# Optimization experiments

Hardware: AMD Instinct MI355X
Metric: run time of the kernel (lower is better)

The kernel has to match this reference:

```python
import jax, jax.numpy as jnp
import numpy as np

H = 16  # headNum
D = 1024  # d_model
DK = D // H


def setup_inputs() -> dict:
    key = jax.random.key(0)
    ks = jax.random.split(key, 11)
    B, S = 2, 2048
    scale = 1.0 / np.sqrt(D)
    inp = {
        'query': jax.random.normal(ks[0], (B, S, D), jnp.float32),
        'key':   jax.random.normal(ks[1], (B, S, D), jnp.float32),
        'value': jax.random.normal(ks[2], (B, S, D), jnp.float32),
        # nn.Linear params: W is [out, in], y = x @ W.T + b
        'Wq': jax.random.normal(ks[3], (D, D), jnp.float32) * scale,
        'bq': jnp.zeros((D,), jnp.float32),
        'Wk': jax.random.normal(ks[4], (D, D), jnp.float32) * scale,
        'bk': jnp.zeros((D,), jnp.float32),
        'Wv': jax.random.normal(ks[5], (D, D), jnp.float32) * scale,
        'bv': jnp.zeros((D,), jnp.float32),
        'Wo': jax.random.normal(ks[6], (D, D), jnp.float32) * scale,
        'bo': jnp.zeros((D,), jnp.float32),
    }
    return inp


def reference(query, key, value, Wq, bq, Wk, bk, Wv, bv, Wo, bo):
    B, S, _ = query.shape
    # projections (torch Linear: x @ W.T + b), split heads -> [B, H, S, DK]
    q = (query @ Wq.T + bq).reshape(B, S, H, DK).transpose(0, 2, 1, 3)
    k = (key   @ Wk.T + bk).reshape(B, S, H, DK).transpose(0, 2, 1, 3)
    v = (value @ Wv.T + bv).reshape(B, S, H, DK).transpose(0, 2, 1, 3)
    # scores [B, H, S, S] = Q K^T / sqrt(d_k)  (fully materialized, as in source)
    scores = jnp.einsum('bhqd,bhkd->bhqk', q, k) * (DK ** -0.5)
    p_attn = jax.nn.softmax(scores, axis=-1)  # dropout = identity (eval)
    x = jnp.einsum('bhqk,bhkd->bhqd', p_attn, v)
    x = x.transpose(0, 2, 1, 3).reshape(B, S, H * DK)
    return x @ Wo.T + bo
```

## Files before the change

### kernel.cpp

```cpp
#include <hip/hip_runtime.h>

#define BATCH 2
#define SEQ   2048
#define NH    16
#define DK    64
#define DM    1024
#define MROWS 4096
#define NX    4194304
#define NW    1048576

typedef __attribute__((ext_vector_type(8))) short bf16x8;
typedef __attribute__((ext_vector_type(4))) short bf16x4;
typedef __attribute__((ext_vector_type(4))) float f32x4;
typedef __attribute__((ext_vector_type(4))) unsigned short us16x4;
typedef __attribute__((ext_vector_type(2))) unsigned int u32x2;

#if __has_builtin(__builtin_amdgcn_mfma_f32_16x16x16bf16_1k)
#define MFMA16(a, b, c) __builtin_amdgcn_mfma_f32_16x16x16bf16_1k(a, b, c, 0, 0, 0)
#else
#define MFMA16(a, b, c) (c)
#endif

__device__ __forceinline__ unsigned short f2bf(float f) {
  unsigned int u = __builtin_bit_cast(unsigned int, f);
  u += 0x7FFFu + ((u >> 16) & 1u);
  return (unsigned short)(u >> 16);
}

__device__ __forceinline__ unsigned int pkbf(float hi, float lo) {
#if __has_builtin(__builtin_amdgcn_perm)
  return __builtin_amdgcn_perm(__builtin_bit_cast(unsigned int, hi),
                               __builtin_bit_cast(unsigned int, lo), 0x07060302u);
#else
  return (__builtin_bit_cast(unsigned int, hi) & 0xffff0000u) |
         (__builtin_bit_cast(unsigned int, lo) >> 16);
#endif
}

__device__ __forceinline__ void g2l16(void* lds, const void* g) {
  __builtin_amdgcn_global_load_lds(
      (const __attribute__((address_space(1))) void*)g,
      (__attribute__((address_space(3))) void*)lds, 16, 0, 0);
}

__global__ __launch_bounds__(256) void cast_all(
    const float* __restrict__ q, const float* __restrict__ k, const float* __restrict__ v,
    const float* __restrict__ wq, const float* __restrict__ wk,
    const float* __restrict__ wv, const float* __restrict__ wo,
    unsigned short* __restrict__ dst) {
  size_t e = ((size_t)blockIdx.x * 256 + threadIdx.x) * 4;
  const float* src;
  if      (e < (size_t)NX)        src = q  + e;
  else if (e < (size_t)2*NX)      src = k  + (e - (size_t)NX);
  else if (e < (size_t)3*NX)      src = v  + (e - (size_t)2*NX);
  else if (e < (size_t)3*NX+NW)   src = wq + (e - (size_t)3*NX);
  else if (e < (size_t)3*NX+2*NW) src = wk + (e - (size_t)3*NX-NW);
  else if (e < (size_t)3*NX+3*NW) src = wv + (e - (size_t)3*NX-2*NW);
  else                            src = wo + (e - (size_t)3*NX-3*NW);
  float4 f = *(const float4*)src;
  us16x4 o;
  o[0] = f2bf(f.x); o[1] = f2bf(f.y); o[2] = f2bf(f.z); o[3] = f2bf(f.w);
  *(us16x4*)(dst + e) = o;
}

template <int MODE, int BM>
__global__ __launch_bounds__(256) void gemm_bt(
    const unsigned short* __restrict__ Xbase, const unsigned short* __restrict__ Wbase,
    const float* __restrict__ b0, const float* __restrict__ b1, const float* __restrict__ b2,
    unsigned short* __restrict__ qkv_dst, float* __restrict__ fout, float qscale) {
  constexpr int IM = BM / 32;
  constexpr int ASHOTS = (BM * 32) / 2048;
  const int tid  = threadIdx.x;
  const int lane = tid & 63;
  const int w    = tid >> 6;
  const int wm   = w >> 1, wn = w & 1;
  const int x15  = lane & 15, quad = lane >> 4;
  const int row0 = blockIdx.x * BM;
  const int col0 = blockIdx.y * 128;
  const int z    = blockIdx.z;

  const unsigned short* A  = Xbase + (size_t)z * NX;
  const unsigned short* Wp = Wbase + (size_t)z * NW;
  const float* bias = (MODE == 0) ? (z == 0 ? b0 : (z == 1 ? b1 : b2)) : b0;
  const float zs = (MODE == 0 && z == 0) ? qscale : 1.0f;

  __shared__ __align__(16) unsigned short At[2][BM * 32];
  __shared__ __align__(16) unsigned short Bt[2][128 * 32];

  f32x4 acc[IM][4] = {};

  auto stage = [&](int buf, int kt) {
#pragma unroll
    for (int j = 0; j < ASHOTS; ++j) {
      int e = (j * 256 + tid) * 8;
      int r = e >> 5, c = e & 31;
      g2l16(&At[buf][e], A + (size_t)(row0 + r) * DM + kt + c);
    }
#pragma unroll
    for (int j = 0; j < 2; ++j) {
      int e = (j * 256 + tid) * 8;
      int r = e >> 5, c = e & 31;
      g2l16(&Bt[buf][e], Wp + (size_t)(col0 + r) * DM + kt + c);
    }
  };

  stage(0, 0);
  for (int it = 0; it < DM / 32; ++it) {
    const int cur = it & 1;
    __syncthreads();
    if (it + 1 < DM / 32) stage(cur ^ 1, (it + 1) * 32);
    bf16x8 af[IM], bfv[4];
#pragma unroll
    for (int i = 0; i < IM; ++i)
      af[i] = *(const bf16x8*)&At[cur][(wm * (BM / 2) + i * 16 + x15) * 32 + quad * 8];
#pragma unroll
    for (int jn = 0; jn < 4; ++jn)
      bfv[jn] = *(const bf16x8*)&Bt[cur][(wn * 64 + jn * 16 + x15) * 32 + quad * 8];
#pragma unroll
    for (int i = 0; i < IM; ++i)
#pragma unroll
      for (int jn = 0; jn < 4; ++jn)
        acc[i][jn] = __builtin_amdgcn_mfma_f32_16x16x32_bf16(af[i], bfv[jn], acc[i][jn], 0, 0, 0);
  }

#pragma unroll
  for (int jn = 0; jn < 4; ++jn) {
    const int n = col0 + wn * 64 + jn * 16 + x15;
    const float bv = bias[n];
#pragma unroll
    for (int i = 0; i < IM; ++i) {
      const int m0 = row0 + wm * (BM / 2) + i * 16 + quad * 4;
      if (MODE == 0 && z == 2) {
        us16x4 pk;
#pragma unroll
        for (int r = 0; r < 4; ++r) pk[r] = f2bf(acc[i][jn][r] + bv);
        const int b = m0 >> 11, s = m0 & 2047;
        const int h = n >> 6,  dk = n & 63;
        *(us16x4*)&qkv_dst[(size_t)2 * NX + (((size_t)(b * NH + h) * DK + dk) << 11) + s] = pk;
      } else {
#pragma unroll
        for (int r = 0; r < 4; ++r) {
          const int m = m0 + r;
          float val = (acc[i][jn][r] + bv) * zs;
          if (MODE == 0) {
            const int b = m >> 11, s = m & 2047;
            const int h = n >> 6,  dk = n & 63;
            qkv_dst[(size_t)z * NX + (((size_t)(b * NH + h) * SEQ + s) << 6) + dk] = f2bf(val);
          } else {
            fout[(size_t)m * DM + n] = val;
          }
        }
      }
    }
  }
}

__global__ __launch_bounds__(256, 2) void attn(
    const unsigned short* __restrict__ Qb, const unsigned short* __restrict__ Kb,
    const unsigned short* __restrict__ VTb, unsigned short* __restrict__ AO) {
  const int tid  = threadIdx.x;
  const int lane = tid & 63;
  const int w    = tid >> 6;
  const int wq   = w & 1;
  const int ws   = w >> 1;
  const int x15  = lane & 15, quad = lane >> 4;
  const int lin = (int)(blockIdx.x | (blockIdx.y << 4) | (blockIdx.z << 8));
  const int swz = ((lin & 7) << 6) | (lin >> 3);
  const int qt = swz & 15;
  const int h  = (swz >> 4) & 15;
  const int b  = swz >> 8;
  const size_t bh = ((size_t)(b * NH + h)) * SEQ * DK;
  const unsigned short* Q  = Qb  + bh;
  const unsigned short* K  = Kb  + bh;
  const unsigned short* VT = VTb + bh;
  const int q0 = qt * 128;

  __shared__ __align__(16) unsigned short smem[3 * 4096 * 2];
  unsigned short* Kl = smem;
  unsigned short* Vl = smem + 12288;
  float* Ored = (float*)smem;
  __shared__ float lbuf[2][4][128];

  bf16x8 qf[4][2];
#pragma unroll
  for (int qgi = 0; qgi < 4; ++qgi)
#pragma unroll
    for (int ks = 0; ks < 2; ++ks)
      qf[qgi][ks] = *(const bf16x8*)&Q[(size_t)(q0 + wq * 64 + qgi * 16 + x15) * DK + ks * 32 + quad * 8];

  f32x4 po[4][4] = {};
  float pol[4] = {0.f, 0.f, 0.f, 0.f};

  const int sK0 = tid >> 3,          sK1 = (tid + 256) >> 3;
  const int dgK0 = (tid & 7) ^ (sK0 & 7), dgK1 = (tid & 7) ^ (sK1 & 7);

  auto stageKV = [&](int buf, int s0) {
    const int bo = buf * 4096;
    g2l16(&Kl[bo + tid * 8],         K + (size_t)(s0 + sK0) * DK + dgK0 * 8);
    g2l16(&Kl[bo + (tid + 256) * 8], K + (size_t)(s0 + sK1) * DK + dgK1 * 8);
    g2l16(&Vl[bo + tid * 8],         VT + (size_t)sK0 * SEQ + s0 + dgK0 * 8);
    g2l16(&Vl[bo + (tid + 256) * 8], VT + (size_t)sK1 * SEQ + s0 + dgK1 * 8);
  };

  int ca = 0, cb = 1, cc = 2;
  stageKV(0, 0);
  stageKV(1, 64);
  for (int i = 0; i < SEQ / 64; ++i) {
    asm volatile("s_waitcnt vmcnt(4)" ::: "memory");
    __builtin_amdgcn_sched_barrier(0);
    __builtin_amdgcn_s_barrier();
    stageKV(cc, ((i + 2) * 64) & (SEQ - 1));
    const int ko = ca * 4096;

    bf16x8 kf[2][2];
#pragma unroll
    for (int shi = 0; shi < 2; ++shi) {
      const int sh = ws * 2 + shi;
      const int kbase = (sh * 16 + x15) * 8;
      kf[shi][0] = *(const bf16x8*)&Kl[ko + (kbase + ((0 + quad) ^ (x15 & 7))) * 8];
      kf[shi][1] = *(const bf16x8*)&Kl[ko + (kbase + ((4 + quad) ^ (x15 & 7))) * 8];
    }
    bf16x4 vf[2][4];
#pragma unroll
    for (int shi = 0; shi < 2; ++shi)
#pragma unroll
      for (int nt = 0; nt < 4; ++nt) {
        const int d = nt * 16 + x15;
        const int sg = ((ws * 2 + shi) * 2 + (quad >> 1)) ^ (d & 7);
        vf[shi][nt] = *(const bf16x4*)&Vl[ko + (d * 8 + sg) * 8 + (quad & 1) * 4];
      }

#pragma unroll
    for (int shi = 0; shi < 2; ++shi) {
#pragma unroll
      for (int qgi = 0; qgi < 4; ++qgi) {
        f32x4 sacc = {};
        sacc = __builtin_amdgcn_mfma_f32_16x16x32_bf16(kf[shi][0], qf[qgi][0], sacc, 0, 0, 0);
        sacc = __builtin_amdgcn_mfma_f32_16x16x32_bf16(kf[shi][1], qf[qgi][1], sacc, 0, 0, 0);
        float p0 = __builtin_amdgcn_exp2f(sacc[0]);
        float p1 = __builtin_amdgcn_exp2f(sacc[1]);
        float p2 = __builtin_amdgcn_exp2f(sacc[2]);
        float p3 = __builtin_amdgcn_exp2f(sacc[3]);
        pol[qgi] += (p0 + p1) + (p2 + p3);
        u32x2 uu;
        uu[0] = pkbf(p1, p0);
        uu[1] = pkbf(p3, p2);
        bf16x4 pf = __builtin_bit_cast(bf16x4, uu);
#pragma unroll
        for (int nt = 0; nt < 4; ++nt)
          po[qgi][nt] = MFMA16(vf[shi][nt], pf, po[qgi][nt]);
      }
    }
    int t = ca; ca = cb; cb = cc; cc = t;
  }

#pragma unroll
  for (int qgi = 0; qgi < 4; ++qgi)
    lbuf[ws][quad][wq * 64 + qgi * 16 + x15] = pol[qgi];
  __syncthreads();

  const int qq = tid >> 2;
  const int d0 = (tid & 3) * 16;
#pragma unroll
  for (int rw = 0; rw < 2; ++rw) {
    if (wq == rw) {
#pragma unroll
      for (int qgi = 0; qgi < 4; ++qgi)
#pragma unroll
        for (int nt = 0; nt < 4; ++nt)
          *(f32x4*)&Ored[(ws * 64 + qgi * 16 + x15) * 68 + nt * 16 + quad * 4] = po[qgi][nt];
    }
    __syncthreads();
    float ls = 0.f;
#pragma unroll
    for (int w2 = 0; w2 < 2; ++w2)
#pragma unroll
      for (int qd = 0; qd < 4; ++qd)
        ls += lbuf[w2][qd][rw * 64 + qq];
    const float inv = 1.0f / ls;
    const size_t orow = ((size_t)(b * SEQ + q0 + rw * 64 + qq)) * DM + h * DK + d0;
#pragma unroll
    for (int c = 0; c < 4; ++c) {
      f32x4 sa = *(const f32x4*)&Ored[(0 * 64 + qq) * 68 + d0 + c * 4];
      f32x4 sb = *(const f32x4*)&Ored[(1 * 64 + qq) * 68 + d0 + c * 4];
      us16x4 pk;
#pragma unroll
      for (int r = 0; r < 4; ++r) pk[r] = f2bf((sa[r] + sb[r]) * inv);
      *(us16x4*)&AO[orow + c * 4] = pk;
    }
    __syncthreads();
  }
}

extern "C" void kernel_launch(void* const* d_in, const int* in_sizes, int n_in,
                              void* d_out, int out_size, void* d_ws, size_t ws_size,
                              hipStream_t stream) {
  const float* q  = (const float*)d_in[0];
  const float* k  = (const float*)d_in[1];
  const float* v  = (const float*)d_in[2];
  const float* wq = (const float*)d_in[3];
  const float* bq = (const float*)d_in[4];
  const float* wk = (const float*)d_in[5];
  const float* bk = (const float*)d_in[6];
  const float* wv = (const float*)d_in[7];
  const float* bv = (const float*)d_in[8];
  const float* wo = (const float*)d_in[9];
  const float* bo = (const float*)d_in[10];
  float* out = (float*)d_out;

  unsigned short* ws = (unsigned short*)d_ws;
  unsigned short* Xq = ws;
  unsigned short* Wb = ws + (size_t)3 * NX;
  unsigned short* Qb = ws + (size_t)3 * NX + 4 * NW;
  unsigned short* AO = Qb + (size_t)3 * NX;

  const float qscale = 0.125f * 1.4426950408889634f;

  cast_all<<<16384, 256, 0, stream>>>(q, k, v, wq, wk, wv, wo, ws);
  gemm_bt<0, 128><<<dim3(32, 8, 3), 256, 0, stream>>>(Xq, Wb, bq, bk, bv, Qb, nullptr, qscale);
  attn<<<dim3(16, 16, 2), 256, 0, stream>>>(Qb, Qb + (size_t)NX, Qb + (size_t)2 * NX, AO);
  gemm_bt<1, 64><<<dim3(64, 8, 1), 256, 0, stream>>>(AO, Wb + (size_t)3 * NW, bo, bo, bo,
                                                     nullptr, out, 1.0f);
}
```

Measured before the change: 223.6 us.

## Vectorize GEMM epilogue via swapped MFMA operands and use 128-key double-buffered attention tiles

The projection GEMM swaps the MFMA A/B operands for Q, K and output modes, so each lane holds four consecutive output columns and can write them with one vector store instead of four scalar ones. The V path keeps the original layout because it writes transposed. The attention kernel moves from a triple-buffered 64-key pipeline to double-buffered 128-key tiles, halving the number of barriers per sequence. The cost is a full vmcnt(0) wait each iteration, more registers for K/V fragments, and larger shared memory, which may cut occupancy or overlap.

```diff
diff --git a/kernel.cpp b/kernel.cpp
--- a/kernel.cpp
+++ b/kernel.cpp
@@ -83,6 +83,7 @@
   const unsigned short* Wp = Wbase + (size_t)z * NW;
   const float* bias = (MODE == 0) ? (z == 0 ? b0 : (z == 1 ? b1 : b2)) : b0;
   const float zs = (MODE == 0 && z == 0) ? qscale : 1.0f;
+  const bool swp = (MODE == 1) || (MODE == 0 && z < 2);
 
   __shared__ __align__(16) unsigned short At[2][BM * 32];
   __shared__ __align__(16) unsigned short Bt[2][128 * 32];
@@ -116,40 +117,58 @@
 #pragma unroll
     for (int jn = 0; jn < 4; ++jn)
       bfv[jn] = *(const bf16x8*)&Bt[cur][(wn * 64 + jn * 16 + x15) * 32 + quad * 8];
-#pragma unroll
-    for (int i = 0; i < IM; ++i)
-#pragma unroll
-      for (int jn = 0; jn < 4; ++jn)
-        acc[i][jn] = __builtin_amdgcn_mfma_f32_16x16x32_bf16(af[i], bfv[jn], acc[i][jn], 0, 0, 0);
+    if (swp) {
+#pragma unroll
+      for (int i = 0; i < IM; ++i)
+#pragma unroll
+        for (int jn = 0; jn < 4; ++jn)
+          acc[i][jn] = __builtin_amdgcn_mfma_f32_16x16x32_bf16(bfv[jn], af[i], acc[i][jn], 0, 0, 0);
+    } else {
+#pragma unroll
+      for (int i = 0; i < IM; ++i)
+#pragma unroll
+        for (int jn = 0; jn < 4; ++jn)
+          acc[i][jn] = __builtin_amdgcn_mfma_f32_16x16x32_bf16(af[i], bfv[jn], acc[i][jn], 0, 0, 0);
+    }
   }
 
-#pragma unroll
-  for (int jn = 0; jn < 4; ++jn) {
-    const int n = col0 + wn * 64 + jn * 16 + x15;
-    const float bv = bias[n];
-#pragma unroll
-    for (int i = 0; i < IM; ++i) {
-      const int m0 = row0 + wm * (BM / 2) + i * 16 + quad * 4;
-      if (MODE == 0 && z == 2) {
+  if (swp) {
+#pragma unroll
+    for (int jn = 0; jn < 4; ++jn) {
+      const int n0 = col0 + wn * 64 + jn * 16 + quad * 4;
+      const f32x4 bv4 = *(const f32x4*)&bias[n0];
+#pragma unroll
+      for (int i = 0; i < IM; ++i) {
+        const int m = row0 + wm * (BM / 2) + i * 16 + x15;
+        if (MODE == 0) {
+          us16x4 pk;
+#pragma unroll
+          for (int r = 0; r < 4; ++r) pk[r] = f2bf((acc[i][jn][r] + bv4[r]) * zs);
+          const int b = m >> 11, s = m & 2047;
+          const int h = n0 >> 6, dk = n0 & 63;
+          *(us16x4*)&qkv_dst[(size_t)z * NX + (((size_t)(b * NH + h) * SEQ + s) << 6) + dk] = pk;
+        } else {
+          f32x4 o;
+#pragma unroll
+          for (int r = 0; r < 4; ++r) o[r] = acc[i][jn][r] + bv4[r];
+          *(f32x4*)&fout[(size_t)m * DM + n0] = o;
+        }
+      }
+    }
+  } else {
+#pragma unroll
+    for (int jn = 0; jn < 4; ++jn) {
+      const int n = col0 + wn * 64 + jn * 16 + x15;
+      const float bv = bias[n];
+#pragma unroll
+      for (int i = 0; i < IM; ++i) {
+        const int m0 = row0 + wm * (BM / 2) + i * 16 + quad * 4;
         us16x4 pk;
 #pragma unroll
         for (int r = 0; r < 4; ++r) pk[r] = f2bf(acc[i][jn][r] + bv);
         const int b = m0 >> 11, s = m0 & 2047;
         const int h = n >> 6,  dk = n & 63;
         *(us16x4*)&qkv_dst[(size_t)2 * NX + (((size_t)(b * NH + h) * DK + dk) << 11) + s] = pk;
-      } else {
-#pragma unroll
-        for (int r = 0; r < 4; ++r) {
-          const int m = m0 + r;
-          float val = (acc[i][jn][r] + bv) * zs;
-          if (MODE == 0) {
-            const int b = m >> 11, s = m & 2047;
-            const int h = n >> 6,  dk = n & 63;
-            qkv_dst[(size_t)z * NX + (((size_t)(b * NH + h) * SEQ + s) << 6) + dk] = f2bf(val);
-          } else {
-            fout[(size_t)m * DM + n] = val;
-          }
-        }
       }
     }
   }
@@ -175,9 +194,9 @@
   const unsigned short* VT = VTb + bh;
   const int q0 = qt * 128;
 
-  __shared__ __align__(16) unsigned short smem[3 * 4096 * 2];
+  __shared__ __align__(16) unsigned short smem[4 * 8192];
   unsigned short* Kl = smem;
-  unsigned short* Vl = smem + 12288;
+  unsigned short* Vl = smem + 16384;
   float* Ored = (float*)smem;
   __shared__ float lbuf[2][4][128];
 
@@ -191,47 +210,54 @@
   f32x4 po[4][4] = {};
   float pol[4] = {0.f, 0.f, 0.f, 0.f};
 
-  const int sK0 = tid >> 3,          sK1 = (tid + 256) >> 3;
-  const int dgK0 = (tid & 7) ^ (sK0 & 7), dgK1 = (tid & 7) ^ (sK1 & 7);
-
   auto stageKV = [&](int buf, int s0) {
-    const int bo = buf * 4096;
-    g2l16(&Kl[bo + tid * 8],         K + (size_t)(s0 + sK0) * DK + dgK0 * 8);
-    g2l16(&Kl[bo + (tid + 256) * 8], K + (size_t)(s0 + sK1) * DK + dgK1 * 8);
-    g2l16(&Vl[bo + tid * 8],         VT + (size_t)sK0 * SEQ + s0 + dgK0 * 8);
-    g2l16(&Vl[bo + (tid + 256) * 8], VT + (size_t)sK1 * SEQ + s0 + dgK1 * 8);
+    const int bo = buf * 8192;
+#pragma unroll
+    for (int j = 0; j < 4; ++j) {
+      const int L = tid + j * 256;
+      const int s = L >> 3, js = L & 7;
+      const int dg = js ^ (s & 7);
+      g2l16(&Kl[bo + L * 8], K + (size_t)(s0 + s) * DK + dg * 8);
+    }
+#pragma unroll
+    for (int j = 0; j < 4; ++j) {
+      const int L = tid + j * 256;
+      const int d = L >> 4, sgs = L & 15;
+      const int sg = sgs ^ (d & 7);
+      g2l16(&Vl[bo + L * 8], VT + (size_t)d * SEQ + s0 + sg * 8);
+    }
   };
 
-  int ca = 0, cb = 1, cc = 2;
   stageKV(0, 0);
-  stageKV(1, 64);
-  for (int i = 0; i < SEQ / 64; ++i) {
-    asm volatile("s_waitcnt vmcnt(4)" ::: "memory");
+  for (int i = 0; i < SEQ / 128; ++i) {
+    const int cur = i & 1;
+    asm volatile("s_waitcnt vmcnt(0)" ::: "memory");
     __builtin_amdgcn_sched_barrier(0);
     __builtin_amdgcn_s_barrier();
-    stageKV(cc, ((i + 2) * 64) & (SEQ - 1));
-    const int ko = ca * 4096;
-
-    bf16x8 kf[2][2];
-#pragma unroll
-    for (int shi = 0; shi < 2; ++shi) {
-      const int sh = ws * 2 + shi;
+    if (i + 1 < SEQ / 128) stageKV(cur ^ 1, (i + 1) * 128);
+    const int ko = cur * 8192;
+
+    bf16x8 kf[4][2];
+#pragma unroll
+    for (int shi = 0; shi < 4; ++shi) {
+      const int sh = ws * 4 + shi;
       const int kbase = (sh * 16 + x15) * 8;
       kf[shi][0] = *(const bf16x8*)&Kl[ko + (kbase + ((0 + quad) ^ (x15 & 7))) * 8];
       kf[shi][1] = *(const bf16x8*)&Kl[ko + (kbase + ((4 + quad) ^ (x15 & 7))) * 8];
     }
-    bf16x4 vf[2][4];
-#pragma unroll
-    for (int shi = 0; shi < 2; ++shi)
+    bf16x4 vf[4][4];
+#pragma unroll
+    for (int shi = 0; shi < 4; ++shi)
 #pragma unroll
       for (int nt = 0; nt < 4; ++nt) {
         const int d = nt * 16 + x15;
-        const int sg = ((ws * 2 + shi) * 2 + (quad >> 1)) ^ (d & 7);
-        vf[shi][nt] = *(const bf16x4*)&Vl[ko + (d * 8 + sg) * 8 + (quad & 1) * 4];
+        const int sgw = (ws * 4 + shi) * 2 + (quad >> 1);
+        const int sgs = sgw ^ (d & 7);
+        vf[shi][nt] = *(const bf16x4*)&Vl[ko + (d * 16 + sgs) * 8 + (quad & 1) * 4];
       }
 
 #pragma unroll
-    for (int shi = 0; shi < 2; ++shi) {
+    for (int shi = 0; shi < 4; ++shi) {
 #pragma unroll
       for (int qgi = 0; qgi < 4; ++qgi) {
         f32x4 sacc = {};
@@ -251,7 +277,6 @@
           po[qgi][nt] = MFMA16(vf[shi][nt], pf, po[qgi][nt]);
       }
     }
-    int t = ca; ca = cb; cb = cc; cc = t;
   }
 
 #pragma unroll
```

Result: slower. 237.1 us (+6.1%).
